# Performance work log

Measured on AMD Instinct MI355X. Metric: run time of the kernel, lower is better.

The kernel has to match this reference:

```python
import jax, jax.numpy as jnp
import numpy as np

IGNORE_INDEX = -100
BETA = 0.1

def setup_inputs() -> dict:
    key = jax.random.key(0)
    k1, k2, k3 = jax.random.split(key, 3)
    B2, T, H, V = 4, 512, 4096, 32000  # B2 = 2*num_pairs (chosen then rejected)
    x = jax.random.normal(k1, (B2, T, H), dtype=jnp.float32)
    target = jax.random.randint(k2, (B2, T), 0, V, dtype=jnp.int64)
    W = jax.random.normal(k3, (V, H), dtype=jnp.float32) * (1.0 / np.sqrt(H))
    return {"x": x, "target": target, "W": W}

def _avg_and_per_token_logps(x, W, target):
    # fused linear + log-softmax + target gather (math of the Liger chunked kernel)
    logits = jnp.einsum('bth,vh->btv', x, W).astype(jnp.float32)  # [B2,T,V]
    logps = jax.nn.log_softmax(logits, axis=-1)
    mask = (target != IGNORE_INDEX)
    labels = jnp.where(mask, target, 0)
    per_tok = jnp.take_along_axis(logps, labels[..., None], axis=-1)[..., 0]
    per_tok = per_tok * mask  # [B2,T]
    avg = per_tok.sum(-1) / mask.sum(-1).astype(jnp.float32)  # [B2]
    return avg, per_tok, mask

def reference(x, target, W):
    B2 = x.shape[0]
    B = B2 // 2
    avg, per_tok, mask = _avg_and_per_token_logps(x, W, target)
    chosen_logps, rejected_logps = avg[:B], avg[B:]
    # reference model: same weights, detached (no_grad in Liger)
    ref_chosen = jax.lax.stop_gradient(chosen_logps)
    ref_rejected = jax.lax.stop_gradient(rejected_logps)
    logits_diff = BETA * ((chosen_logps - ref_chosen) - (rejected_logps - ref_rejected))
    pref_loss = -jax.nn.log_sigmoid(logits_diff).sum() / B
    # chosen-half NLL (compute_nll_loss=True)
    nll = -(per_tok[:B]).sum() / mask[:B].sum().astype(jnp.float32)
    return pref_loss + nll
```

## Files before the change

kernel.cpp:

```cpp
#include <hip/hip_runtime.h>


#define IGNORE_INDEX (-100)

typedef __attribute__((ext_vector_type(8))) short short8;
typedef __attribute__((ext_vector_type(4))) float f32x4;

constexpr int Ktot = 4096;
constexpr int Mtot = 1024;
constexpr int Vtot = 32000;
constexpr int NTILES = 250;
constexpr long long NX = (long long)Mtot * Ktot;
constexpr long long NW = (long long)Vtot * Ktot;

__device__ __forceinline__ unsigned pack2_bf16(float a, float b) {
    unsigned ua = __float_as_uint(a);
    unsigned ub = __float_as_uint(b);
    ua += 0x7FFFu + ((ua >> 16) & 1u);
    ub += 0x7FFFu + ((ub >> 16) & 1u);
    return (ua >> 16) | (ub & 0xFFFF0000u);
}

__device__ __forceinline__ void load_lds_16(const void* g, void* l) {
    __builtin_amdgcn_global_load_lds(
        (const __attribute__((address_space(1))) unsigned int*)g,
        (__attribute__((address_space(3))) unsigned int*)l, 16, 0, 0);
}

__global__ __launch_bounds__(256)
void convert_to_bf16(const float* __restrict__ X, const float* __restrict__ W,
                     unsigned short* __restrict__ Xb, unsigned short* __restrict__ Wb)
{
    long long i = ((long long)blockIdx.x * 256 + threadIdx.x) * 8;
    const float* src;
    unsigned short* dst;
    long long off;
    if (i < NX) { src = X; dst = Xb; off = i; }
    else        { src = W; dst = Wb; off = i - NX; }
    float4 v0 = *(const float4*)(src + off);
    float4 v1 = *(const float4*)(src + off + 4);
    uint4 p;
    p.x = pack2_bf16(v0.x, v0.y);
    p.y = pack2_bf16(v0.z, v0.w);
    p.z = pack2_bf16(v1.x, v1.y);
    p.w = pack2_bf16(v1.z, v1.w);
    *(uint4*)(dst + off) = p;
}

__global__ __launch_bounds__(256, 2)
void gemm_lse_bf16(const unsigned short* __restrict__ Xb,
                   const unsigned short* __restrict__ Wb,
                   const int* __restrict__ tgt2,
                   float* __restrict__ ws_sum, float* __restrict__ ws_tl)
{
    int b = blockIdx.x;
    int xcd  = b & 7;
    int j    = b >> 3;
    int mt_b = j & 7;
    int grp  = j >> 3;
    int nt_b = xcd + 8 * grp;
    if (nt_b >= NTILES) return;

    const int m0 = mt_b * 128;
    const int n0 = nt_b * 128;

    __shared__ __align__(16) unsigned short As[128 * 32];
    __shared__ __align__(16) unsigned short Bs[128 * 32];

    const int tid  = threadIdx.x;
    const int srow = tid >> 2;
    const int sseg = tid & 3;
    const int gseg = sseg ^ (srow & 3);

    const unsigned short* aG = Xb + (size_t)(m0 + srow) * Ktot + gseg * 8;
    const unsigned short* bG = Wb + (size_t)(n0 + srow) * Ktot + gseg * 8;
    unsigned short* aL = As + srow * 32 + sseg * 8;
    unsigned short* bL = Bs + srow * 32 + sseg * 8;

    const int lane = tid & 63;
    const int wid  = tid >> 6;
    const int wm = (wid >> 1) * 64, wn = (wid & 1) * 64;
    const int quad = lane >> 4, lq = lane & 15;
    const int rseg = (quad ^ (lq & 3)) * 8;

    f32x4 acc[4][4];
#pragma unroll
    for (int i = 0; i < 4; i++)
#pragma unroll
        for (int jj = 0; jj < 4; jj++)
            acc[i][jj] = (f32x4){0.f, 0.f, 0.f, 0.f};

    constexpr size_t halfjump = (size_t)64 * Ktot;

    for (int kk = 0; kk < Ktot; kk += 32) {
        __syncthreads();
        load_lds_16(aG + kk,            aL);
        load_lds_16(aG + kk + halfjump, aL + 64 * 32);
        load_lds_16(bG + kk,            bL);
        load_lds_16(bG + kk + halfjump, bL + 64 * 32);
        __syncthreads();

        short8 af[4], bf[4];
#pragma unroll
        for (int mt = 0; mt < 4; mt++)
            af[mt] = *(const short8*)&As[(wm + mt * 16 + lq) * 32 + rseg];
#pragma unroll
        for (int nt = 0; nt < 4; nt++)
            bf[nt] = *(const short8*)&Bs[(wn + nt * 16 + lq) * 32 + rseg];

#pragma unroll
        for (int mt = 0; mt < 4; mt++)
#pragma unroll
            for (int nt = 0; nt < 4; nt++)
                acc[mt][nt] = __builtin_amdgcn_mfma_f32_16x16x32_bf16(
                    af[mt], bf[nt], acc[mt][nt], 0, 0, 0);
    }

#pragma unroll
    for (int mt = 0; mt < 4; mt++) {
#pragma unroll
        for (int rr = 0; rr < 4; rr++) {
            float s = __expf(acc[mt][0][rr]) + __expf(acc[mt][1][rr]) +
                      __expf(acc[mt][2][rr]) + __expf(acc[mt][3][rr]);
            s += __shfl_xor(s, 1);
            s += __shfl_xor(s, 2);
            s += __shfl_xor(s, 4);
            s += __shfl_xor(s, 8);
            const int row = m0 + wm + mt * 16 + quad * 4 + rr;
            if (lq == 0) atomicAdd(&ws_sum[row], s);
            const int tv = tgt2[2 * row];
#pragma unroll
            for (int nt = 0; nt < 4; nt++) {
                const int col = n0 + wn + nt * 16 + lq;
                if (col == tv) ws_tl[row] = acc[mt][nt][rr];
            }
        }
    }
}

__global__ __launch_bounds__(256, 2)
void dpo_gemm_lse_fb(const float* __restrict__ X, const float* __restrict__ W,
                     const int* __restrict__ tgt2,
                     float* __restrict__ ws_sum, float* __restrict__ ws_tl)
{
    int b = blockIdx.x;
    int xcd  = b & 7;
    int j    = b >> 3;
    int mt_b = j & 7;
    int grp  = j >> 3;
    int nt_b = xcd + 8 * grp;
    if (nt_b >= NTILES) return;

    const int m0 = mt_b * 128;
    const int n0 = nt_b * 128;

    __shared__ __align__(16) unsigned As[128 * 16];
    __shared__ __align__(16) unsigned Bs[128 * 16];

    const int tid = threadIdx.x;
    const int r = tid >> 1, h = tid & 1;

    const float* aptr = X + (size_t)(m0 + r) * Ktot + h * 16;
    const float* bptr = W + (size_t)(n0 + r) * Ktot + h * 16;

    const int lane = tid & 63;
    const int wid  = tid >> 6;
    const int wm = (wid >> 1) * 64, wn = (wid & 1) * 64;
    const int quad = lane >> 4, lq = lane & 15;

    f32x4 acc[4][4];
#pragma unroll
    for (int i = 0; i < 4; i++)
#pragma unroll
        for (int jj = 0; jj < 4; jj++)
            acc[i][jj] = (f32x4){0.f, 0.f, 0.f, 0.f};

    for (int kk = 0; kk < Ktot; kk += 32) {
        const float4* ap = (const float4*)(aptr + kk);
        const float4* bp = (const float4*)(bptr + kk);
        float4 a0 = ap[0], a1 = ap[1], a2 = ap[2], a3 = ap[3];
        float4 b0 = bp[0], b1 = bp[1], b2 = bp[2], b3 = bp[3];

        __syncthreads();

        uint4 pa0, pa1, pb0, pb1;
        pa0.x = pack2_bf16(a0.x, a0.y); pa0.y = pack2_bf16(a0.z, a0.w);
        pa0.z = pack2_bf16(a1.x, a1.y); pa0.w = pack2_bf16(a1.z, a1.w);
        pa1.x = pack2_bf16(a2.x, a2.y); pa1.y = pack2_bf16(a2.z, a2.w);
        pa1.z = pack2_bf16(a3.x, a3.y); pa1.w = pack2_bf16(a3.z, a3.w);
        pb0.x = pack2_bf16(b0.x, b0.y); pb0.y = pack2_bf16(b0.z, b0.w);
        pb0.z = pack2_bf16(b1.x, b1.y); pb0.w = pack2_bf16(b1.z, b1.w);
        pb1.x = pack2_bf16(b2.x, b2.y); pb1.y = pack2_bf16(b2.z, b2.w);
        pb1.z = pack2_bf16(b3.x, b3.y); pb1.w = pack2_bf16(b3.z, b3.w);

        *(uint4*)&As[r * 16 + h * 8]     = pa0;
        *(uint4*)&As[r * 16 + h * 8 + 4] = pa1;
        *(uint4*)&Bs[r * 16 + h * 8]     = pb0;
        *(uint4*)&Bs[r * 16 + h * 8 + 4] = pb1;

        __syncthreads();

        short8 af[4], bf[4];
#pragma unroll
        for (int mt = 0; mt < 4; mt++)
            af[mt] = __builtin_bit_cast(short8,
                *(const uint4*)&As[(wm + mt * 16 + lq) * 16 + quad * 4]);
#pragma unroll
        for (int nt = 0; nt < 4; nt++)
            bf[nt] = __builtin_bit_cast(short8,
                *(const uint4*)&Bs[(wn + nt * 16 + lq) * 16 + quad * 4]);

#pragma unroll
        for (int mt = 0; mt < 4; mt++)
#pragma unroll
            for (int nt = 0; nt < 4; nt++)
                acc[mt][nt] = __builtin_amdgcn_mfma_f32_16x16x32_bf16(
                    af[mt], bf[nt], acc[mt][nt], 0, 0, 0);
    }

#pragma unroll
    for (int mt = 0; mt < 4; mt++) {
#pragma unroll
        for (int rr = 0; rr < 4; rr++) {
            float s = __expf(acc[mt][0][rr]) + __expf(acc[mt][1][rr]) +
                      __expf(acc[mt][2][rr]) + __expf(acc[mt][3][rr]);
            s += __shfl_xor(s, 1);
            s += __shfl_xor(s, 2);
            s += __shfl_xor(s, 4);
            s += __shfl_xor(s, 8);
            const int row = m0 + wm + mt * 16 + quad * 4 + rr;
            if (lq == 0) atomicAdd(&ws_sum[row], s);
            const int tv = tgt2[2 * row];
#pragma unroll
            for (int nt = 0; nt < 4; nt++) {
                const int col = n0 + wn + nt * 16 + lq;
                if (col == tv) ws_tl[row] = acc[mt][nt][rr];
            }
        }
    }
}

__global__ void dpo_finalize(const float* __restrict__ ws_sum,
                             const float* __restrict__ ws_tl,
                             const int* __restrict__ tgt2,
                             float* __restrict__ out)
{
    __shared__ float sred[4];
    __shared__ float cred[4];
    float s = 0.f, c = 0.f;
    for (int i = threadIdx.x; i < 1024; i += 256) {
        const int tv = tgt2[2 * i];
        if (tv != IGNORE_INDEX) {
            s += ws_tl[i] - logf(ws_sum[i]);
            c += 1.f;
        }
    }
#pragma unroll
    for (int o = 32; o > 0; o >>= 1) {
        s += __shfl_down(s, o);
        c += __shfl_down(c, o);
    }
    const int wv = threadIdx.x >> 6, lane = threadIdx.x & 63;
    if (lane == 0) { sred[wv] = s; cred[wv] = c; }
    __syncthreads();
    if (threadIdx.x == 0) {
        const float st = sred[0] + sred[1] + sred[2] + sred[3];
        const float ct = cred[0] + cred[1] + cred[2] + cred[3];
        out[0] = 0.69314718055994531f - st / ct;
    }
}

extern "C" void kernel_launch(void* const* d_in, const int* in_sizes, int n_in,
                              void* d_out, int out_size, void* d_ws, size_t ws_size,
                              hipStream_t stream) {
    const float* X    = (const float*)d_in[0];
    const int*   tgt2 = (const int*)d_in[1];
    const float* W    = (const float*)d_in[2];
    float* out = (float*)d_out;

    float* ws_sum = (float*)d_ws;
    float* ws_tl  = ws_sum + 1024;
    unsigned short* Xb = (unsigned short*)(ws_tl + 1024);
    unsigned short* Wb = Xb + NX;

    const size_t need = 2048 * sizeof(float) + (size_t)(NX + NW) * 2;

    hipMemsetAsync(d_ws, 0, 2048 * sizeof(float), stream);
    if (ws_size >= need) {
        const int conv_blocks = (int)((NX + NW) / 8 / 256);
        convert_to_bf16<<<conv_blocks, 256, 0, stream>>>(X, W, Xb, Wb);
        gemm_lse_bf16<<<2048, 256, 0, stream>>>(Xb, Wb, tgt2, ws_sum, ws_tl);
    } else {
        dpo_gemm_lse_fb<<<2048, 256, 0, stream>>>(X, W, tgt2, ws_sum, ws_tl);
    }
    dpo_finalize<<<1, 256, 0, stream>>>(ws_sum, ws_tl, tgt2, out);
}
```

Before: 1.021 ms.

## Fuse W fp32-to-bf16 conversion into GEMM with double-buffered register prefetch

Drops the separate pass that converts the whole 32000x4096 W matrix to bf16. Only X is pre-converted now; the GEMM loads fp32 W tiles into registers two k-steps ahead, packs them to bf16, and writes them into double-buffered LDS. X tiles are prefetched into the other LDS buffer with direct-to-LDS loads and manual s_waitcnt control. This removes a large read-write of W through HBM but doubles the W bytes each GEMM block reads and adds conversion ALU work and register pressure inside the main loop.

```diff
diff --git a/kernel.cpp b/kernel.cpp
--- a/kernel.cpp
+++ b/kernel.cpp
@@ -11,7 +11,6 @@
 constexpr int Vtot = 32000;
 constexpr int NTILES = 250;
 constexpr long long NX = (long long)Mtot * Ktot;
-constexpr long long NW = (long long)Vtot * Ktot;
 
 __device__ __forceinline__ unsigned pack2_bf16(float a, float b) {
     unsigned ua = __float_as_uint(a);
@@ -28,30 +27,71 @@
 }
 
 __global__ __launch_bounds__(256)
-void convert_to_bf16(const float* __restrict__ X, const float* __restrict__ W,
-                     unsigned short* __restrict__ Xb, unsigned short* __restrict__ Wb)
+void convert_x(const float* __restrict__ X, unsigned short* __restrict__ Xb)
 {
     long long i = ((long long)blockIdx.x * 256 + threadIdx.x) * 8;
-    const float* src;
-    unsigned short* dst;
-    long long off;
-    if (i < NX) { src = X; dst = Xb; off = i; }
-    else        { src = W; dst = Wb; off = i - NX; }
-    float4 v0 = *(const float4*)(src + off);
-    float4 v1 = *(const float4*)(src + off + 4);
+    float4 v0 = *(const float4*)(X + i);
+    float4 v1 = *(const float4*)(X + i + 4);
     uint4 p;
     p.x = pack2_bf16(v0.x, v0.y);
     p.y = pack2_bf16(v0.z, v0.w);
     p.z = pack2_bf16(v1.x, v1.y);
     p.w = pack2_bf16(v1.z, v1.w);
-    *(uint4*)(dst + off) = p;
-}
+    *(uint4*)(Xb + i) = p;
+}
+
+#define KSTEP(T, P, V0, V1, V2, V3, VMSTR, IA, IB) do {                         \
+    asm volatile("s_waitcnt " VMSTR ::: "memory");                              \
+    {                                                                           \
+        uint2 q0, q1, q2, q3;                                                   \
+        q0.x = pack2_bf16(V0.x, V0.y); q0.y = pack2_bf16(V0.z, V0.w);           \
+        q1.x = pack2_bf16(V1.x, V1.y); q1.y = pack2_bf16(V1.z, V1.w);           \
+        q2.x = pack2_bf16(V2.x, V2.y); q2.y = pack2_bf16(V2.z, V2.w);           \
+        q3.x = pack2_bf16(V3.x, V3.y); q3.y = pack2_bf16(V3.z, V3.w);           \
+        *(uint2*)&Bs[P][bw0 +    0] = q0;                                       \
+        *(uint2*)&Bs[P][bw0 + 1024] = q1;                                       \
+        *(uint2*)&Bs[P][bw0 + 2048] = q2;                                       \
+        *(uint2*)&Bs[P][bw0 + 3072] = q3;                                       \
+    }                                                                           \
+    if (IA) {                                                                   \
+        load_lds_16(aG + (size_t)((T) + 1) * 32,         &As[(P) ^ 1][aL]);     \
+        load_lds_16(aG + (size_t)((T) + 1) * 32 + ahalf, &As[(P) ^ 1][2048 + aL]); \
+    }                                                                           \
+    asm volatile("" ::: "memory");       \
+    if (IB) {                                                                   \
+        V0 = *(const float4*)(bG + (size_t)((T) + 2) * 32 + 0 * brj);           \
+        V1 = *(const float4*)(bG + (size_t)((T) + 2) * 32 + 1 * brj);           \
+        V2 = *(const float4*)(bG + (size_t)((T) + 2) * 32 + 2 * brj);           \
+        V3 = *(const float4*)(bG + (size_t)((T) + 2) * 32 + 3 * brj);           \
+    }                                                                           \
+    asm volatile("s_waitcnt lgkmcnt(0)" ::: "memory");                          \
+    __builtin_amdgcn_s_barrier();                                               \
+    asm volatile("" ::: "memory");                                              \
+    {                                                                           \
+        short8 af[4], bf[4];                                                    \
+        _Pragma("unroll")                                                       \
+        for (int mt = 0; mt < 4; mt++)                                          \
+            af[mt] = *(const short8*)&As[P][(wm + mt * 16 + lq) * 32 + rseg];   \
+        _Pragma("unroll")                                                       \
+        for (int nt = 0; nt < 4; nt++)                                          \
+            bf[nt] = *(const short8*)&Bs[P][(wn + nt * 16 + lq) * 32 + rseg];   \
+        _Pragma("unroll")                                                       \
+        for (int mt = 0; mt < 4; mt++)                                          \
+            _Pragma("unroll")                                                   \
+            for (int nt = 0; nt < 4; nt++)                                      \
+                acc[mt][nt] = __builtin_amdgcn_mfma_f32_16x16x32_bf16(          \
+                    af[mt], bf[nt], acc[mt][nt], 0, 0, 0);                      \
+    }                                                                           \
+    asm volatile("s_waitcnt lgkmcnt(0)" ::: "memory");                          \
+    __builtin_amdgcn_s_barrier();                                               \
+    asm volatile("" ::: "memory");                                              \
+} while (0)
 
 __global__ __launch_bounds__(256, 2)
-void gemm_lse_bf16(const unsigned short* __restrict__ Xb,
-                   const unsigned short* __restrict__ Wb,
-                   const int* __restrict__ tgt2,
-                   float* __restrict__ ws_sum, float* __restrict__ ws_tl)
+void gemm_lse_fused(const unsigned short* __restrict__ Xb,
+                    const float* __restrict__ W,
+                    const int* __restrict__ tgt2,
+                    float* __restrict__ ws_sum, float* __restrict__ ws_tl)
 {
     int b = blockIdx.x;
     int xcd  = b & 7;
@@ -64,18 +104,22 @@
     const int m0 = mt_b * 128;
     const int n0 = nt_b * 128;
 
-    __shared__ __align__(16) unsigned short As[128 * 32];
-    __shared__ __align__(16) unsigned short Bs[128 * 32];
-
-    const int tid  = threadIdx.x;
-    const int srow = tid >> 2;
-    const int sseg = tid & 3;
-    const int gseg = sseg ^ (srow & 3);
-
-    const unsigned short* aG = Xb + (size_t)(m0 + srow) * Ktot + gseg * 8;
-    const unsigned short* bG = Wb + (size_t)(n0 + srow) * Ktot + gseg * 8;
-    unsigned short* aL = As + srow * 32 + sseg * 8;
-    unsigned short* bL = Bs + srow * 32 + sseg * 8;
+    __shared__ __align__(16) unsigned short As[2][128 * 32];
+    __shared__ __align__(16) unsigned short Bs[2][128 * 32];
+
+    const int tid = threadIdx.x;
+
+    const int arow  = tid >> 2;
+    const int gsegA = (tid & 3) ^ (arow & 3);
+    const unsigned short* aG = Xb + (size_t)(m0 + arow) * Ktot + gsegA * 8;
+    const int aL = tid * 8;
+    constexpr size_t ahalf = (size_t)64 * Ktot;
+
+    const int tr = tid >> 3;
+    const int tg = tid & 7;
+    const float* bG = W + (size_t)(n0 + tr) * Ktot + tg * 4;
+    const int bw0 = tr * 32 + (((tg >> 1) ^ (tr & 3)) * 8) + ((tg & 1) * 4);
+    constexpr size_t brj = (size_t)32 * Ktot;
 
     const int lane = tid & 63;
     const int wid  = tid >> 6;
@@ -90,133 +134,27 @@
         for (int jj = 0; jj < 4; jj++)
             acc[i][jj] = (f32x4){0.f, 0.f, 0.f, 0.f};
 
-    constexpr size_t halfjump = (size_t)64 * Ktot;
-
-    for (int kk = 0; kk < Ktot; kk += 32) {
-        __syncthreads();
-        load_lds_16(aG + kk,            aL);
-        load_lds_16(aG + kk + halfjump, aL + 64 * 32);
-        load_lds_16(bG + kk,            bL);
-        load_lds_16(bG + kk + halfjump, bL + 64 * 32);
-        __syncthreads();
-
-        short8 af[4], bf[4];
-#pragma unroll
-        for (int mt = 0; mt < 4; mt++)
-            af[mt] = *(const short8*)&As[(wm + mt * 16 + lq) * 32 + rseg];
-#pragma unroll
-        for (int nt = 0; nt < 4; nt++)
-            bf[nt] = *(const short8*)&Bs[(wn + nt * 16 + lq) * 32 + rseg];
-
-#pragma unroll
-        for (int mt = 0; mt < 4; mt++)
-#pragma unroll
-            for (int nt = 0; nt < 4; nt++)
-                acc[mt][nt] = __builtin_amdgcn_mfma_f32_16x16x32_bf16(
-                    af[mt], bf[nt], acc[mt][nt], 0, 0, 0);
-    }
-
-#pragma unroll
-    for (int mt = 0; mt < 4; mt++) {
-#pragma unroll
-        for (int rr = 0; rr < 4; rr++) {
-            float s = __expf(acc[mt][0][rr]) + __expf(acc[mt][1][rr]) +
-                      __expf(acc[mt][2][rr]) + __expf(acc[mt][3][rr]);
-            s += __shfl_xor(s, 1);
-            s += __shfl_xor(s, 2);
-            s += __shfl_xor(s, 4);
-            s += __shfl_xor(s, 8);
-            const int row = m0 + wm + mt * 16 + quad * 4 + rr;
-            if (lq == 0) atomicAdd(&ws_sum[row], s);
-            const int tv = tgt2[2 * row];
-#pragma unroll
-            for (int nt = 0; nt < 4; nt++) {
-                const int col = n0 + wn + nt * 16 + lq;
-                if (col == tv) ws_tl[row] = acc[mt][nt][rr];
-            }
-        }
-    }
-}
-
-__global__ __launch_bounds__(256, 2)
-void dpo_gemm_lse_fb(const float* __restrict__ X, const float* __restrict__ W,
-                     const int* __restrict__ tgt2,
-                     float* __restrict__ ws_sum, float* __restrict__ ws_tl)
-{
-    int b = blockIdx.x;
-    int xcd  = b & 7;
-    int j    = b >> 3;
-    int mt_b = j & 7;
-    int grp  = j >> 3;
-    int nt_b = xcd + 8 * grp;
-    if (nt_b >= NTILES) return;
-
-    const int m0 = mt_b * 128;
-    const int n0 = nt_b * 128;
-
-    __shared__ __align__(16) unsigned As[128 * 16];
-    __shared__ __align__(16) unsigned Bs[128 * 16];
-
-    const int tid = threadIdx.x;
-    const int r = tid >> 1, h = tid & 1;
-
-    const float* aptr = X + (size_t)(m0 + r) * Ktot + h * 16;
-    const float* bptr = W + (size_t)(n0 + r) * Ktot + h * 16;
-
-    const int lane = tid & 63;
-    const int wid  = tid >> 6;
-    const int wm = (wid >> 1) * 64, wn = (wid & 1) * 64;
-    const int quad = lane >> 4, lq = lane & 15;
-
-    f32x4 acc[4][4];
-#pragma unroll
-    for (int i = 0; i < 4; i++)
-#pragma unroll
-        for (int jj = 0; jj < 4; jj++)
-            acc[i][jj] = (f32x4){0.f, 0.f, 0.f, 0.f};
-
-    for (int kk = 0; kk < Ktot; kk += 32) {
-        const float4* ap = (const float4*)(aptr + kk);
-        const float4* bp = (const float4*)(bptr + kk);
-        float4 a0 = ap[0], a1 = ap[1], a2 = ap[2], a3 = ap[3];
-        float4 b0 = bp[0], b1 = bp[1], b2 = bp[2], b3 = bp[3];
-
-        __syncthreads();
-
-        uint4 pa0, pa1, pb0, pb1;
-        pa0.x = pack2_bf16(a0.x, a0.y); pa0.y = pack2_bf16(a0.z, a0.w);
-        pa0.z = pack2_bf16(a1.x, a1.y); pa0.w = pack2_bf16(a1.z, a1.w);
-        pa1.x = pack2_bf16(a2.x, a2.y); pa1.y = pack2_bf16(a2.z, a2.w);
-        pa1.z = pack2_bf16(a3.x, a3.y); pa1.w = pack2_bf16(a3.z, a3.w);
-        pb0.x = pack2_bf16(b0.x, b0.y); pb0.y = pack2_bf16(b0.z, b0.w);
-        pb0.z = pack2_bf16(b1.x, b1.y); pb0.w = pack2_bf16(b1.z, b1.w);
-        pb1.x = pack2_bf16(b2.x, b2.y); pb1.y = pack2_bf16(b2.z, b2.w);
-        pb1.z = pack2_bf16(b3.x, b3.y); pb1.w = pack2_bf16(b3.z, b3.w);
-
-        *(uint4*)&As[r * 16 + h * 8]     = pa0;
-        *(uint4*)&As[r * 16 + h * 8 + 4] = pa1;
-        *(uint4*)&Bs[r * 16 + h * 8]     = pb0;
-        *(uint4*)&Bs[r * 16 + h * 8 + 4] = pb1;
-
-        __syncthreads();
-
-        short8 af[4], bf[4];
-#pragma unroll
-        for (int mt = 0; mt < 4; mt++)
-            af[mt] = __builtin_bit_cast(short8,
-                *(const uint4*)&As[(wm + mt * 16 + lq) * 16 + quad * 4]);
-#pragma unroll
-        for (int nt = 0; nt < 4; nt++)
-            bf[nt] = __builtin_bit_cast(short8,
-                *(const uint4*)&Bs[(wn + nt * 16 + lq) * 16 + quad * 4]);
-
-#pragma unroll
-        for (int mt = 0; mt < 4; mt++)
-#pragma unroll
-            for (int nt = 0; nt < 4; nt++)
-                acc[mt][nt] = __builtin_amdgcn_mfma_f32_16x16x32_bf16(
-                    af[mt], bf[nt], acc[mt][nt], 0, 0, 0);
-    }
+    float4 va0, va1, va2, va3, vb0, vb1, vb2, vb3;
+    va0 = *(const float4*)(bG + 0 * brj);
+    va1 = *(const float4*)(bG + 1 * brj);
+    va2 = *(const float4*)(bG + 2 * brj);
+    va3 = *(const float4*)(bG + 3 * brj);
+    asm volatile("" ::: "memory");
+    load_lds_16(aG,         &As[0][aL]);
+    load_lds_16(aG + ahalf, &As[0][2048 + aL]);
+    asm volatile("" ::: "memory");
+    vb0 = *(const float4*)(bG + 32 + 0 * brj);
+    vb1 = *(const float4*)(bG + 32 + 1 * brj);
+    vb2 = *(const float4*)(bG + 32 + 2 * brj);
+    vb3 = *(const float4*)(bG + 32 + 3 * brj);
+    asm volatile("" ::: "memory");
+
+    for (int t = 0; t < 126; t += 2) {
+        KSTEP(t,     0, va0, va1, va2, va3, "vmcnt(4)", true,  true);
+        KSTEP(t + 1, 1, vb0, vb1, vb2, vb3, "vmcnt(4)", true,  true);
+    }
+    KSTEP(126, 0, va0, va1, va2, va3, "vmcnt(4)", true,  false);
+    KSTEP(127, 1, vb0, vb1, vb2, vb3, "vmcnt(0)", false, false);
 
 #pragma unroll
     for (int mt = 0; mt < 4; mt++) {
@@ -281,17 +219,9 @@
     float* ws_sum = (float*)d_ws;
     float* ws_tl  = ws_sum + 1024;
     unsigned short* Xb = (unsigned short*)(ws_tl + 1024);
-    unsigned short* Wb = Xb + NX;
-
-    const size_t need = 2048 * sizeof(float) + (size_t)(NX + NW) * 2;
 
     hipMemsetAsync(d_ws, 0, 2048 * sizeof(float), stream);
-    if (ws_size >= need) {
-        const int conv_blocks = (int)((NX + NW) / 8 / 256);
-        convert_to_bf16<<<conv_blocks, 256, 0, stream>>>(X, W, Xb, Wb);
-        gemm_lse_bf16<<<2048, 256, 0, stream>>>(Xb, Wb, tgt2, ws_sum, ws_tl);
-    } else {
-        dpo_gemm_lse_fb<<<2048, 256, 0, stream>>>(X, W, tgt2, ws_sum, ws_tl);
-    }
+    convert_x<<<(int)(NX / 8 / 256), 256, 0, stream>>>(X, Xb);
+    gemm_lse_fused<<<2048, 256, 0, stream>>>(Xb, W, tgt2, ws_sum, ws_tl);
     dpo_finalize<<<1, 256, 0, stream>>>(ws_sum, ws_tl, tgt2, out);
 }
```

New measurement: 1.063 ms. 4.1% more time.

## Replace bf16 GEMM with 256x256-tile, 8-phase double-buffered pipelined kernel

Applied to the files above, without the earlier changes.

Replaces the 128x128 single-buffered bf16 GEMM with a 512-thread kernel that computes 256x256 tiles with K-step 64. LDS is double-buffered and global-to-LDS loads are interleaved with MFMA phases using explicit barriers, waitcnt and setprio. Workgroups are remapped per XCD for locality, and an XOR swizzle avoids LDS bank conflicts. The aim is to hide memory latency and raise MFMA utilisation, at the cost of heavy register and LDS use, which may limit occupancy. The larger tiles also mean fewer workgroups (500) for the GPU to balance across its compute units.

```diff
diff --git a/kernel.cpp b/kernel.cpp
--- a/kernel.cpp
+++ b/kernel.cpp
@@ -9,9 +9,9 @@
 constexpr int Ktot = 4096;
 constexpr int Mtot = 1024;
 constexpr int Vtot = 32000;
-constexpr int NTILES = 250;
 constexpr long long NX = (long long)Mtot * Ktot;
 constexpr long long NW = (long long)Vtot * Ktot;
+constexpr int NWG = 4 * 125;
 
 __device__ __forceinline__ unsigned pack2_bf16(float a, float b) {
     unsigned ua = __float_as_uint(a);
@@ -47,77 +47,122 @@
     *(uint4*)(dst + off) = p;
 }
 
-__global__ __launch_bounds__(256, 2)
-void gemm_lse_bf16(const unsigned short* __restrict__ Xb,
-                   const unsigned short* __restrict__ Wb,
-                   const int* __restrict__ tgt2,
-                   float* __restrict__ ws_sum, float* __restrict__ ws_tl)
+
+#define STG(OP, BUF, HALF, TILE) do {                                          \
+    const unsigned short* _s = s##OP##0 + (size_t)(HALF) * (128 * 4096)        \
+                               + (size_t)(TILE) * 64;                          \
+    unsigned short* _d = d##OP + (BUF) * 16384 + (HALF) * 8192;                \
+    load_lds_16(_s,             _d);                                           \
+    load_lds_16(_s + 64 * 4096, _d + 4096);                                    \
+} while (0)
+
+#define B1() do { __builtin_amdgcn_s_barrier();                                \
+    asm volatile("s_waitcnt lgkmcnt(0)" ::: "memory");                         \
+    __builtin_amdgcn_sched_barrier(0); } while (0)
+
+#define B2() do { __builtin_amdgcn_s_barrier();                                \
+    __builtin_amdgcn_sched_barrier(0); } while (0)
+
+#define B2VM(S) do { asm volatile("s_waitcnt " S ::: "memory");                \
+    __builtin_amdgcn_s_barrier();                                              \
+    __builtin_amdgcn_sched_barrier(0); } while (0)
+
+#define LD_AF(BUF, MTB) do { _Pragma("unroll")                                 \
+    for (int _m = 0; _m < 4; _m++) {                                           \
+        af[_m][0] = *(const short8*)&As[BUF][rowA + ((MTB) + _m) * 1024 + sw0];\
+        af[_m][1] = *(const short8*)&As[BUF][rowA + ((MTB) + _m) * 1024 + sw1];\
+    } } while (0)
+
+#define LD_BF(BUF, NTB) do { _Pragma("unroll")                                 \
+    for (int _n = 0; _n < 2; _n++) {                                           \
+        bf[(NTB) + _n][0] = *(const short8*)&Bs[BUF][rowB + ((NTB) + _n) * 1024 + sw0]; \
+        bf[(NTB) + _n][1] = *(const short8*)&Bs[BUF][rowB + ((NTB) + _n) * 1024 + sw1]; \
+    } } while (0)
+
+#define MF(MTB, NTB) do { __builtin_amdgcn_s_setprio(1);                       \
+    _Pragma("unroll") for (int _m = 0; _m < 4; _m++)                           \
+    _Pragma("unroll") for (int _n = 0; _n < 2; _n++)                           \
+    _Pragma("unroll") for (int _k = 0; _k < 2; _k++)                           \
+        acc[(MTB) + _m][(NTB) + _n] = __builtin_amdgcn_mfma_f32_16x16x32_bf16( \
+            af[_m][_k], bf[(NTB) + _n][_k], acc[(MTB) + _m][(NTB) + _n], 0, 0, 0); \
+    __builtin_amdgcn_s_setprio(0); } while (0)
+
+#define ITER(T1, T2, T3, FULL, VM4) do {                                       \
+     LD_AF(0, 0); LD_BF(0, 0); STG(A, 1, 0, (T1));                    \
+    B1(); MF(0, 0); B2();                                                      \
+     LD_BF(0, 2); STG(A, 1, 1, (T1));                                 \
+    B1(); MF(0, 2); B2();                                                      \
+     LD_AF(0, 4); if (FULL) STG(B, 0, 0, (T2));                       \
+    B1(); MF(4, 0); B2();                                                      \
+     if (FULL) STG(B, 0, 1, (T2));                                    \
+    B1(); MF(4, 2); B2VM(VM4);                                                 \
+     LD_AF(1, 0); LD_BF(1, 0); if (FULL) STG(A, 0, 0, (T2));          \
+    B1(); MF(0, 0); B2();                                                      \
+     LD_BF(1, 2); if (FULL) STG(A, 0, 1, (T2));                       \
+    B1(); MF(0, 2); B2();                                                      \
+     LD_AF(1, 4); if (FULL) STG(B, 1, 0, (T3));                       \
+    B1(); MF(4, 0); B2();                                                      \
+     if (FULL) STG(B, 1, 1, (T3));                                    \
+    B1(); MF(4, 2);                                                            \
+    if (FULL) { B2VM("vmcnt(4)"); } else { B2(); }                             \
+} while (0)
+
+__global__ __launch_bounds__(512, 2)
+void gemm_lse_8ph(const unsigned short* __restrict__ Xb,
+                  const unsigned short* __restrict__ Wb,
+                  const int* __restrict__ tgt2,
+                  float* __restrict__ ws_sum, float* __restrict__ ws_tl)
 {
     int b = blockIdx.x;
-    int xcd  = b & 7;
-    int j    = b >> 3;
-    int mt_b = j & 7;
-    int grp  = j >> 3;
-    int nt_b = xcd + 8 * grp;
-    if (nt_b >= NTILES) return;
-
-    const int m0 = mt_b * 128;
-    const int n0 = nt_b * 128;
-
-    __shared__ __align__(16) unsigned short As[128 * 32];
-    __shared__ __align__(16) unsigned short Bs[128 * 32];
-
-    const int tid  = threadIdx.x;
-    const int srow = tid >> 2;
-    const int sseg = tid & 3;
-    const int gseg = sseg ^ (srow & 3);
-
-    const unsigned short* aG = Xb + (size_t)(m0 + srow) * Ktot + gseg * 8;
-    const unsigned short* bG = Wb + (size_t)(n0 + srow) * Ktot + gseg * 8;
-    unsigned short* aL = As + srow * 32 + sseg * 8;
-    unsigned short* bL = Bs + srow * 32 + sseg * 8;
-
-    const int lane = tid & 63;
-    const int wid  = tid >> 6;
-    const int wm = (wid >> 1) * 64, wn = (wid & 1) * 64;
-    const int quad = lane >> 4, lq = lane & 15;
-    const int rseg = (quad ^ (lq & 3)) * 8;
-
-    f32x4 acc[4][4];
-#pragma unroll
-    for (int i = 0; i < 4; i++)
-#pragma unroll
-        for (int jj = 0; jj < 4; jj++)
-            acc[i][jj] = (f32x4){0.f, 0.f, 0.f, 0.f};
-
-    constexpr size_t halfjump = (size_t)64 * Ktot;
-
-    for (int kk = 0; kk < Ktot; kk += 32) {
-        __syncthreads();
-        load_lds_16(aG + kk,            aL);
-        load_lds_16(aG + kk + halfjump, aL + 64 * 32);
-        load_lds_16(bG + kk,            bL);
-        load_lds_16(bG + kk + halfjump, bL + 64 * 32);
-        __syncthreads();
-
-        short8 af[4], bf[4];
-#pragma unroll
-        for (int mt = 0; mt < 4; mt++)
-            af[mt] = *(const short8*)&As[(wm + mt * 16 + lq) * 32 + rseg];
-#pragma unroll
-        for (int nt = 0; nt < 4; nt++)
-            bf[nt] = *(const short8*)&Bs[(wn + nt * 16 + lq) * 32 + rseg];
-
-#pragma unroll
-        for (int mt = 0; mt < 4; mt++)
-#pragma unroll
-            for (int nt = 0; nt < 4; nt++)
-                acc[mt][nt] = __builtin_amdgcn_mfma_f32_16x16x32_bf16(
-                    af[mt], bf[nt], acc[mt][nt], 0, 0, 0);
-    }
-
-#pragma unroll
-    for (int mt = 0; mt < 4; mt++) {
+    int xcd = b & 7, bi = b >> 3;
+    int wg = (xcd < 4 ? xcd * 63 : 252 + (xcd - 4) * 62) + bi;
+    const int mt_b = wg & 3, nt_b = wg >> 2;
+    const int m0 = mt_b * 256, n0 = nt_b * 256;
+
+    __shared__ __align__(16) unsigned short As[2][256 * 64];
+    __shared__ __align__(16) unsigned short Bs[2][256 * 64];
+
+    const int tid = threadIdx.x;
+    const int l = tid & 63, w = tid >> 6;
+
+    const int srow = w * 8 + (l >> 3);
+    const int gseg = (l & 7) ^ ((l >> 3) & 7);
+    const unsigned short* sA0 = Xb + (size_t)(m0 + srow) * 4096 + gseg * 8;
+    const unsigned short* sB0 = Wb + (size_t)(n0 + srow) * 4096 + gseg * 8;
+    unsigned short* dA = &As[0][0] + tid * 8;
+    unsigned short* dB = &Bs[0][0] + tid * 8;
+
+    const int wr = w >> 2, wc = w & 3;
+    const int quad = l >> 4, lq = l & 15;
+    const int rowA = (wr * 128 + lq) * 64;
+    const int rowB = (wc * 64 + lq) * 64;
+    const int sw0 = ((0 + quad) ^ (lq & 7)) * 8;
+    const int sw1 = ((4 + quad) ^ (lq & 7)) * 8;
+
+    f32x4 acc[8][4];
+#pragma unroll
+    for (int i = 0; i < 8; i++)
+#pragma unroll
+        for (int j = 0; j < 4; j++)
+            acc[i][j] = (f32x4){0.f, 0.f, 0.f, 0.f};
+
+    short8 af[4][2];
+    short8 bf[4][2];
+
+    STG(A, 0, 0, 0); STG(A, 0, 1, 0);
+    STG(B, 0, 0, 0); STG(B, 0, 1, 0);
+    STG(B, 1, 0, 1); STG(B, 1, 1, 1);
+    asm volatile("s_waitcnt vmcnt(4)" ::: "memory");
+    __builtin_amdgcn_s_barrier();
+    __builtin_amdgcn_sched_barrier(0);
+
+    for (int i = 0; i < 31; i++) {
+        ITER(2 * i + 1, 2 * i + 2, 2 * i + 3, true, "vmcnt(4)");
+    }
+    ITER(63, 0, 0, false, "vmcnt(0)");
+
+#pragma unroll
+    for (int mt = 0; mt < 8; mt++) {
 #pragma unroll
         for (int rr = 0; rr < 4; rr++) {
             float s = __expf(acc[mt][0][rr]) + __expf(acc[mt][1][rr]) +
@@ -126,12 +171,12 @@
             s += __shfl_xor(s, 2);
             s += __shfl_xor(s, 4);
             s += __shfl_xor(s, 8);
-            const int row = m0 + wm + mt * 16 + quad * 4 + rr;
+            const int row = m0 + wr * 128 + mt * 16 + quad * 4 + rr;
             if (lq == 0) atomicAdd(&ws_sum[row], s);
             const int tv = tgt2[2 * row];
 #pragma unroll
             for (int nt = 0; nt < 4; nt++) {
-                const int col = n0 + wn + nt * 16 + lq;
+                const int col = n0 + wc * 64 + nt * 16 + lq;
                 if (col == tv) ws_tl[row] = acc[mt][nt][rr];
             }
         }
@@ -149,13 +194,13 @@
     int mt_b = j & 7;
     int grp  = j >> 3;
     int nt_b = xcd + 8 * grp;
-    if (nt_b >= NTILES) return;
+    if (nt_b >= 250) return;
 
     const int m0 = mt_b * 128;
     const int n0 = nt_b * 128;
 
-    __shared__ __align__(16) unsigned As[128 * 16];
-    __shared__ __align__(16) unsigned Bs[128 * 16];
+    __shared__ __align__(16) unsigned Asf[128 * 16];
+    __shared__ __align__(16) unsigned Bsf[128 * 16];
 
     const int tid = threadIdx.x;
     const int r = tid >> 1, h = tid & 1;
@@ -193,29 +238,29 @@
         pb1.x = pack2_bf16(b2.x, b2.y); pb1.y = pack2_bf16(b2.z, b2.w);
         pb1.z = pack2_bf16(b3.x, b3.y); pb1.w = pack2_bf16(b3.z, b3.w);
 
-        *(uint4*)&As[r * 16 + h * 8]     = pa0;
-        *(uint4*)&As[r * 16 + h * 8 + 4] = pa1;
-        *(uint4*)&Bs[r * 16 + h * 8]     = pb0;
-        *(uint4*)&Bs[r * 16 + h * 8 + 4] = pb1;
+        *(uint4*)&Asf[r * 16 + h * 8]     = pa0;
+        *(uint4*)&Asf[r * 16 + h * 8 + 4] = pa1;
+        *(uint4*)&Bsf[r * 16 + h * 8]     = pb0;
+        *(uint4*)&Bsf[r * 16 + h * 8 + 4] = pb1;
 
         __syncthreads();
 
-        short8 af[4], bf[4];
+        short8 af[4], bfv[4];
 #pragma unroll
         for (int mt = 0; mt < 4; mt++)
             af[mt] = __builtin_bit_cast(short8,
-                *(const uint4*)&As[(wm + mt * 16 + lq) * 16 + quad * 4]);
+                *(const uint4*)&Asf[(wm + mt * 16 + lq) * 16 + quad * 4]);
 #pragma unroll
         for (int nt = 0; nt < 4; nt++)
-            bf[nt] = __builtin_bit_cast(short8,
-                *(const uint4*)&Bs[(wn + nt * 16 + lq) * 16 + quad * 4]);
+            bfv[nt] = __builtin_bit_cast(short8,
+                *(const uint4*)&Bsf[(wn + nt * 16 + lq) * 16 + quad * 4]);
 
 #pragma unroll
         for (int mt = 0; mt < 4; mt++)
 #pragma unroll
             for (int nt = 0; nt < 4; nt++)
                 acc[mt][nt] = __builtin_amdgcn_mfma_f32_16x16x32_bf16(
-                    af[mt], bf[nt], acc[mt][nt], 0, 0, 0);
+                    af[mt], bfv[nt], acc[mt][nt], 0, 0, 0);
     }
 
 #pragma unroll
@@ -289,7 +334,7 @@
     if (ws_size >= need) {
         const int conv_blocks = (int)((NX + NW) / 8 / 256);
         convert_to_bf16<<<conv_blocks, 256, 0, stream>>>(X, W, Xb, Wb);
-        gemm_lse_bf16<<<2048, 256, 0, stream>>>(Xb, Wb, tgt2, ws_sum, ws_tl);
+        gemm_lse_8ph<<<NWG, 512, 0, stream>>>(Xb, Wb, tgt2, ws_sum, ws_tl);
     } else {
         dpo_gemm_lse_fb<<<2048, 256, 0, stream>>>(X, W, tgt2, ws_sum, ws_tl);
     }
```

Result: no change. 1.002 ms (-1.9%).
